# Kernel tuning notes

Hardware: AMD Instinct MI355X
Metric: run time of the kernel (lower is better)

The kernel has to match this reference:

```python
import jax, jax.numpy as jnp
import numpy as np

N_SPANS = 4096
EMB_DIM = 384
HEADS = 4
DECAY_LAMBDA = 5.0
THRESHOLD = 0.1
NEG_SLOPE = 0.2  # PyG GATConv default leaky_relu slope


def setup_inputs() -> dict:
    key = jax.random.key(0)
    k1, k2, k3, k4, k5, k6 = jax.random.split(key, 6)
    embeddings = jax.random.normal(k1, (N_SPANS, EMB_DIM), dtype=jnp.float32)
    span_positions = jnp.sort(
        jax.random.randint(k2, (N_SPANS, 2), 0, 100000), axis=1
    ).astype(jnp.int64)
    # GATConv params: lin (no bias), per-head attention vectors, output bias
    glorot = 1.0 / np.sqrt(EMB_DIM)
    W = jax.random.normal(k3, (EMB_DIM, HEADS, EMB_DIM), dtype=jnp.float32) * glorot
    att_src = jax.random.normal(k4, (HEADS, EMB_DIM), dtype=jnp.float32) * glorot
    att_dst = jax.random.normal(k5, (HEADS, EMB_DIM), dtype=jnp.float32) * glorot
    bias = jnp.zeros((EMB_DIM,), dtype=jnp.float32)
    return {
        "embeddings": embeddings,
        "span_positions": span_positions,
        "W": W,
        "att_src": att_src,
        "att_dst": att_dst,
        "bias": bias,
    }


def _adjacency_mask(embeddings):
    # A_ij = cos_sim(e_i, e_j) * exp(-|i - j| / lambda); edges where A > 0.1
    n = embeddings.shape[0]
    en = embeddings / jnp.linalg.norm(embeddings, axis=1, keepdims=True)
    cos_sim = en @ en.T  # [N, N]
    idx = jnp.arange(n, dtype=embeddings.dtype)
    decay = jnp.exp(-jnp.abs(idx[None, :] - idx[:, None]) / DECAY_LAMBDA)
    adj = cos_sim * decay
    # diagonal is 1.0 > threshold, so self-loops (required by GATConv) are present
    return adj > THRESHOLD  # symmetric mask: mask[i, j] == edge j -> i


def reference(embeddings, span_positions, W, att_src, att_dst, bias):
    mask = _adjacency_mask(embeddings)  # [N_dst, N_src]
    # GATConv(heads=4, concat=False): project, per-head additive attention
    x = jnp.einsum("nd,dhe->nhe", embeddings, W)  # [N, H, E]
    a_src = jnp.einsum("nhe,he->nh", x, att_src)  # [N, H]
    a_dst = jnp.einsum("nhe,he->nh", x, att_dst)  # [N, H]
    # logits[i, j, h] for edge j -> i
    logits = jax.nn.leaky_relu(a_dst[:, None, :] + a_src[None, :, :], NEG_SLOPE)
    logits = jnp.where(mask[:, :, None], logits, jnp.float32(-jnp.inf))
    alpha = jax.nn.softmax(logits, axis=1)  # softmax over incoming sources j
    out = jnp.einsum("ijh,jhe->ihe", alpha, x)  # [N, H, E]
    out = out.mean(axis=1) + bias  # concat=False -> mean over heads, then bias
    return out
```

## Files before the change

kernel.cpp:

```cpp
#include <hip/hip_runtime.h>
#include <hip/hip_bf16.h>
#include <math.h>

#define N_SPANS 4096
#define EMB 384
#define HEADS 4
#define HE (HEADS * EMB)
#define BAND 11
#define BW (2 * BAND + 1)

typedef short bf16x8 __attribute__((ext_vector_type(8)));
typedef float f32x4 __attribute__((ext_vector_type(4)));

__device__ __forceinline__ unsigned short f2bf(float f) {
    union { float f; unsigned u; } x; x.f = f;
    unsigned r = x.u + 0x7fffu + ((x.u >> 16) & 1u);
    return (unsigned short)(r >> 16);
}
__device__ __forceinline__ float bf2f(unsigned short u) {
    union { unsigned u; float f; } x; x.u = ((unsigned)u) << 16; return x.f;
}

__device__ __forceinline__ float wave_sum(float v) {
    #pragma unroll
    for (int off = 32; off; off >>= 1) v += __shfl_xor(v, off, 64);
    return v;
}
__device__ __forceinline__ float wave_max(float v) {
    #pragma unroll
    for (int off = 32; off; off >>= 1) v = fmaxf(v, __shfl_xor(v, off, 64));
    return v;
}

__device__ __forceinline__ void gl2lds16(const void* g, void* l) {
    __builtin_amdgcn_global_load_lds(
        (const __attribute__((address_space(1))) void*)(uintptr_t)g,
        (__attribute__((address_space(3))) void*)(unsigned)(uintptr_t)l,
        16, 0, 0);
}

__global__ __launch_bounds__(256) void prep(const float* __restrict__ E,
                                            const float* __restrict__ W,
                                            unsigned short* __restrict__ Ebf,
                                            unsigned short* __restrict__ Wt,
                                            float* __restrict__ invn,
                                            float* __restrict__ Dots,
                                            float* __restrict__ attacc) {
    __shared__ float tile[32][33];
    const int b = blockIdx.x;
    const int tid = threadIdx.x;
    if (b < 1024) {
        const int lane = tid & 63, w = tid >> 6;
        const int n = b * 4 + w;
        const float* er = E + (size_t)n * EMB;
        const int dmax = (n >= N_SPANS - BAND) ? (N_SPANS - 1 - n) : BAND;
        const float* nb[BAND];
        #pragma unroll
        for (int d = 1; d <= BAND; ++d) {
            int j = n + d; if (j > N_SPANS - 1) j = N_SPANS - 1;
            nb[d - 1] = E + (size_t)j * EMB;
        }
        float acc[12];
        #pragma unroll
        for (int d = 0; d < 12; ++d) acc[d] = 0.f;
        float ev[6];
        #pragma unroll
        for (int m = 0; m < 6; ++m) {
            const int k = m * 64 + lane;
            const float v = er[k];
            ev[m] = v;
            acc[0] += v * v;
            #pragma unroll
            for (int d = 1; d <= BAND; ++d) {
                float u = nb[d - 1][k];
                acc[d] += (d <= dmax) ? v * u : 0.f;
            }
        }
        #pragma unroll
        for (int m = 0; m < 6; ++m)
            Ebf[(size_t)n * EMB + m * 64 + lane] = f2bf(ev[m]);
        #pragma unroll
        for (int d = 0; d < 12; ++d) acc[d] = wave_sum(acc[d]);
        float dval = 0.f;
        #pragma unroll
        for (int d = 1; d <= BAND; ++d) if (lane == d) dval = acc[d];
        if (lane >= 1 && lane <= BAND) Dots[(size_t)n * 12 + lane] = dval;
        if (lane == 0) invn[n] = 1.0f / sqrtf(acc[0]);
    } else if (b < 1600) {
        const int t = b - 1024;
        const int n0 = (t % 48) * 32;
        const int k0 = (t / 48) * 32;
        const int tx = tid & 31, ty = tid >> 5;
        #pragma unroll
        for (int q = 0; q < 4; ++q)
            tile[ty + q * 8][tx] = W[(k0 + ty + q * 8) * HE + n0 + tx];
        __syncthreads();
        #pragma unroll
        for (int q = 0; q < 4; ++q)
            Wt[(n0 + ty + q * 8) * EMB + k0 + tx] = f2bf(tile[tx][ty + q * 8]);
    } else {
        const int t = b - 1600;
        ((float4*)attacc)[t * 256 + tid] = make_float4(0.f, 0.f, 0.f, 0.f);
    }
}

__global__ __launch_bounds__(256) void gemm_attn(const unsigned short* __restrict__ Ebf,
                                                 const unsigned short* __restrict__ Wt,
                                                 const float* __restrict__ attS,
                                                 const float* __restrict__ attD,
                                                 unsigned short* __restrict__ Xb,
                                                 float* __restrict__ asrc,
                                                 float* __restrict__ adst) {
    __shared__ unsigned short As[128 * 32];
    __shared__ unsigned short Bs[128 * 32];
    const int tid = threadIdx.x;
    const int lane = tid & 63;
    const int wave = tid >> 6;
    const int m0 = blockIdx.y * 128;
    const int n0 = blockIdx.x * 128;
    const int wr = (wave >> 1) * 64;
    const int wc = (wave & 1) * 64;
    const int quad = lane >> 4;
    const int l16 = lane & 15;

    const char* Ab = (const char*)Ebf + (size_t)(m0 + wave * 32 + (lane >> 2)) * 768 + (lane & 3) * 16;
    const char* Bb = (const char*)Wt  + (size_t)(n0 + wave * 32 + (lane >> 2)) * 768 + (lane & 3) * 16;
    char* AsB = (char*)As + wave * 32 * 64;
    char* BsB = (char*)Bs + wave * 32 * 64;

    f32x4 acc[4][4];
    #pragma unroll
    for (int i = 0; i < 4; ++i)
        #pragma unroll
        for (int j = 0; j < 4; ++j) acc[i][j] = 0.f;

    for (int kt = 0; kt < 12; ++kt) {
        const int kb = kt * 64;
        __syncthreads();
        gl2lds16(Ab + kb,            AsB);
        gl2lds16(Ab + kb + 16 * 768, AsB + 16 * 64);
        gl2lds16(Bb + kb,            BsB);
        gl2lds16(Bb + kb + 16 * 768, BsB + 16 * 64);
        __syncthreads();

        bf16x8 af[4], bfr[4];
        #pragma unroll
        for (int t = 0; t < 4; ++t) {
            af[t]  = *(const bf16x8*)(&As[(wr + t * 16 + l16) * 32 + quad * 8]);
            bfr[t] = *(const bf16x8*)(&Bs[(wc + t * 16 + l16) * 32 + quad * 8]);
        }
        #pragma unroll
        for (int ti = 0; ti < 4; ++ti)
            #pragma unroll
            for (int tj = 0; tj < 4; ++tj)
                acc[ti][tj] = __builtin_amdgcn_mfma_f32_16x16x32_bf16(
                    af[ti], bfr[tj], acc[ti][tj], 0, 0, 0);
    }

    const int hblk = (n0 + wc) / EMB;
    float aS[4], aD[4];
    #pragma unroll
    for (int tj = 0; tj < 4; ++tj) {
        int col = n0 + wc + tj * 16 + l16;
        aS[tj] = attS[col];
        aD[tj] = attD[col];
    }
    #pragma unroll
    for (int ti = 0; ti < 4; ++ti)
        #pragma unroll
        for (int r = 0; r < 4; ++r) {
            float ps = 0.f, pd = 0.f;
            #pragma unroll
            for (int tj = 0; tj < 4; ++tj) {
                float v = acc[ti][tj][r];
                ps += v * aS[tj];
                pd += v * aD[tj];
            }
            #pragma unroll
            for (int off = 1; off < 16; off <<= 1) {
                ps += __shfl_xor(ps, off, 64);
                pd += __shfl_xor(pd, off, 64);
            }
            if (l16 == 0) {
                int row = m0 + wr + ti * 16 + quad * 4 + r;
                atomicAdd(&asrc[row * HEADS + hblk], ps);
                atomicAdd(&adst[row * HEADS + hblk], pd);
            }
        }

    #pragma unroll
    for (int ti = 0; ti < 4; ++ti)
        #pragma unroll
        for (int tj = 0; tj < 4; ++tj) {
            int col = n0 + wc + tj * 16 + l16;
            #pragma unroll
            for (int r = 0; r < 4; ++r) {
                int row = m0 + wr + ti * 16 + quad * 4 + r;
                Xb[row * HE + col] = f2bf(acc[ti][tj][r]);
            }
        }
}

__global__ __launch_bounds__(256) void band_attn(const float* __restrict__ invn,
                                                 const float* __restrict__ Dots,
                                                 const float* __restrict__ asrc,
                                                 const float* __restrict__ adst,
                                                 const unsigned short* __restrict__ Xb,
                                                 const float* __restrict__ bias,
                                                 float* __restrict__ out) {
    __shared__ float sAl[4][BW][4];
    __shared__ int sList[4][24];
    const int tid = threadIdx.x, lane = tid & 63, w = tid >> 6;
    const int i = blockIdx.x * 4 + w;
    const int jo = lane;
    const int j = i - BAND + jo;
    const bool inb = (jo < BW) && (j >= 0) && (j < N_SPANS);
    const int jc = inb ? j : i;

    float dotv = 0.f;
    if (inb) {
        if (jo < BAND)      dotv = Dots[(size_t)j * 12 + (BAND - jo)];
        else if (jo > BAND) dotv = Dots[(size_t)i * 12 + (jo - BAND)];
    }
    bool flag;
    if (jo == BAND) {
        flag = true;
    } else {
        int dd = jo < BAND ? BAND - jo : jo - BAND;
        float a = ((dotv * invn[i]) * invn[jc]) * expf(-(float)dd * 0.2f);
        flag = inb && (a > 0.1f);
    }

    unsigned long long mbits = __ballot(flag);
    const int cnt = __popcll(mbits);
    const int rank = __popcll(mbits & ((1ull << jo) - 1ull));
    if (flag) sList[w][rank] = jo;

    const float4 ad = ((const float4*)adst)[i];
    const float4 as = inb ? ((const float4*)asrc)[jc] : make_float4(0.f, 0.f, 0.f, 0.f);
    float al[4];
    #pragma unroll
    for (int h = 0; h < 4; ++h) {
        float z = (&ad.x)[h] + (&as.x)[h];
        z = (z >= 0.f) ? z : 0.2f * z;
        float lg = flag ? z : -INFINITY;
        float mx = wave_max(lg);
        float ex = flag ? expf(lg - mx) : 0.f;
        float sm = wave_sum(ex);
        al[h] = ex / sm;
    }
    if (flag) *(float4*)&sAl[w][jo][0] = make_float4(al[0], al[1], al[2], al[3]);

    #pragma unroll
    for (int m = 0; m < 6; ++m) {
        const int e = m * 64 + lane;
        float acc = 0.f;
        for (int ii = 0; ii < cnt; ++ii) {
            const int joL = sList[w][ii];
            const int jj = i - BAND + joL;
            const float4 a4 = *(const float4*)&sAl[w][joL][0];
            const unsigned short* xr = Xb + (size_t)jj * HE + e;
            acc += a4.x * bf2f(xr[0])   + a4.y * bf2f(xr[384])
                 + a4.z * bf2f(xr[768]) + a4.w * bf2f(xr[1152]);
        }
        out[i * EMB + e] = 0.25f * acc + bias[e];
    }
}

extern "C" void kernel_launch(void* const* d_in, const int* in_sizes, int n_in,
                              void* d_out, int out_size, void* d_ws, size_t ws_size,
                              hipStream_t stream) {
    const float* E       = (const float*)d_in[0];
    const float* W       = (const float*)d_in[2];
    const float* att_src = (const float*)d_in[3];
    const float* att_dst = (const float*)d_in[4];
    const float* bias    = (const float*)d_in[5];
    float* out = (float*)d_out;

    char* ws = (char*)d_ws;
    unsigned short* Xb  = (unsigned short*)ws;
    unsigned short* Ebf = (unsigned short*)(ws + 12582912);
    unsigned short* Wt  = (unsigned short*)(ws + 15728640);
    float* invn         = (float*)(ws + 16908288);
    float* asrc         = (float*)(ws + 16924672);
    float* adst         = (float*)(ws + 16990208);
    float* Dots         = (float*)(ws + 17055744);

    prep<<<1632, 256, 0, stream>>>(E, W, Ebf, Wt, invn, Dots, asrc );
    gemm_attn<<<dim3(12, 32), 256, 0, stream>>>(Ebf, Wt, att_src, att_dst, Xb, asrc, adst);
    band_attn<<<1024, 256, 0, stream>>>(invn, Dots, asrc, adst, Xb, bias, out);
}
```

Baseline: 109.6 us.

## Interleave heads in projected X layout and vectorize prep dot products

The projected features Xb are now stored as [row][emb][head] instead of [row][head][emb]. The band attention kernel can then fetch all four heads for one element with a single 8-byte ushort4 load instead of four strided 2-byte loads. The prep kernel is also changed to read rows as float4 and store the bf16 copy as ushort4, which cuts its load instruction count. The cost is that the GEMM epilogue now writes with a stride of 4 elements, giving scattered 2-byte stores that coalesce poorly.

```diff
diff --git a/kernel.cpp b/kernel.cpp
--- a/kernel.cpp
+++ b/kernel.cpp
@@ -30,6 +30,9 @@
     #pragma unroll
     for (int off = 32; off; off >>= 1) v = fmaxf(v, __shfl_xor(v, off, 64));
     return v;
+}
+__device__ __forceinline__ float dot4(float4 a, float4 b) {
+    return a.x * b.x + a.y * b.y + a.z * b.z + a.w * b.w;
 }
 
 __device__ __forceinline__ void gl2lds16(const void* g, void* l) {
@@ -52,33 +55,34 @@
     if (b < 1024) {
         const int lane = tid & 63, w = tid >> 6;
         const int n = b * 4 + w;
-        const float* er = E + (size_t)n * EMB;
-        const int dmax = (n >= N_SPANS - BAND) ? (N_SPANS - 1 - n) : BAND;
-        const float* nb[BAND];
+        const float4* er4 = (const float4*)(E + (size_t)n * EMB);
+        const float4* nb4[BAND];
         #pragma unroll
         for (int d = 1; d <= BAND; ++d) {
             int j = n + d; if (j > N_SPANS - 1) j = N_SPANS - 1;
-            nb[d - 1] = E + (size_t)j * EMB;
-        }
+            nb4[d - 1] = (const float4*)(E + (size_t)j * EMB);
+        }
+        const bool lo = (lane < 32);
+        float4 v0 = er4[lane];
+        float4 v1 = make_float4(0.f, 0.f, 0.f, 0.f);
+        if (lo) v1 = er4[64 + lane];
         float acc[12];
-        #pragma unroll
-        for (int d = 0; d < 12; ++d) acc[d] = 0.f;
-        float ev[6];
-        #pragma unroll
-        for (int m = 0; m < 6; ++m) {
-            const int k = m * 64 + lane;
-            const float v = er[k];
-            ev[m] = v;
-            acc[0] += v * v;
-            #pragma unroll
-            for (int d = 1; d <= BAND; ++d) {
-                float u = nb[d - 1][k];
-                acc[d] += (d <= dmax) ? v * u : 0.f;
-            }
-        }
-        #pragma unroll
-        for (int m = 0; m < 6; ++m)
-            Ebf[(size_t)n * EMB + m * 64 + lane] = f2bf(ev[m]);
+        acc[0] = dot4(v0, v0) + dot4(v1, v1);
+        #pragma unroll
+        for (int d = 1; d <= BAND; ++d) {
+            float4 u0 = nb4[d - 1][lane];
+            float4 u1 = make_float4(0.f, 0.f, 0.f, 0.f);
+            if (lo) u1 = nb4[d - 1][64 + lane];
+            acc[d] = dot4(v0, u0) + dot4(v1, u1);
+        }
+        ushort4 c0;
+        c0.x = f2bf(v0.x); c0.y = f2bf(v0.y); c0.z = f2bf(v0.z); c0.w = f2bf(v0.w);
+        ((ushort4*)(Ebf + (size_t)n * EMB))[lane] = c0;
+        if (lo) {
+            ushort4 c1;
+            c1.x = f2bf(v1.x); c1.y = f2bf(v1.y); c1.z = f2bf(v1.z); c1.w = f2bf(v1.w);
+            ((ushort4*)(Ebf + (size_t)n * EMB))[64 + lane] = c1;
+        }
         #pragma unroll
         for (int d = 0; d < 12; ++d) acc[d] = wave_sum(acc[d]);
         float dval = 0.f;
@@ -158,6 +162,7 @@
     }
 
     const int hblk = (n0 + wc) / EMB;
+    const int e0   = (n0 + wc) % EMB;
     float aS[4], aD[4];
     #pragma unroll
     for (int tj = 0; tj < 4; ++tj) {
@@ -192,11 +197,11 @@
     for (int ti = 0; ti < 4; ++ti)
         #pragma unroll
         for (int tj = 0; tj < 4; ++tj) {
-            int col = n0 + wc + tj * 16 + l16;
+            int e = e0 + tj * 16 + l16;
             #pragma unroll
             for (int r = 0; r < 4; ++r) {
                 int row = m0 + wr + ti * 16 + quad * 4 + r;
-                Xb[row * HE + col] = f2bf(acc[ti][tj][r]);
+                Xb[((size_t)row * EMB + e) * HEADS + hblk] = f2bf(acc[ti][tj][r]);
             }
         }
 }
@@ -251,6 +256,7 @@
     }
     if (flag) *(float4*)&sAl[w][jo][0] = make_float4(al[0], al[1], al[2], al[3]);
 
+    const ushort4* X4 = (const ushort4*)Xb;
     #pragma unroll
     for (int m = 0; m < 6; ++m) {
         const int e = m * 64 + lane;
@@ -259,9 +265,9 @@
             const int joL = sList[w][ii];
             const int jj = i - BAND + joL;
             const float4 a4 = *(const float4*)&sAl[w][joL][0];
-            const unsigned short* xr = Xb + (size_t)jj * HE + e;
-            acc += a4.x * bf2f(xr[0])   + a4.y * bf2f(xr[384])
-                 + a4.z * bf2f(xr[768]) + a4.w * bf2f(xr[1152]);
+            const ushort4 xv = X4[(size_t)jj * EMB + e];
+            acc += a4.x * bf2f(xv.x) + a4.y * bf2f(xv.y)
+                 + a4.z * bf2f(xv.z) + a4.w * bf2f(xv.w);
         }
         out[i * EMB + e] = 0.25f * acc + bias[e];
     }
```

After: 115.3 us. 1.05x slower.
